# Kernel tuning notes

Measured on AMD Instinct MI355X. Metric: run time of the kernel, lower is better.

The kernel has to match this reference:

```python
import jax, jax.numpy as jnp
import numpy as np

P = 2000
C, H, W = 512, 192, 336
STRIDE = 8
IMG_H, IMG_W = H * STRIDE, W * STRIDE


def setup_inputs() -> dict:
    key = jax.random.key(0)
    kx, kxs, kys = jax.random.split(key, 3)
    x = jax.random.normal(kx, (1, C, H, W), dtype=jnp.float32)
    # valid boxes: x1<=x2 in [0, IMG_W), y1<=y2 in [0, IMG_H)
    xs = jnp.sort(jax.random.randint(kxs, (P, 2), 0, IMG_W), axis=1).astype(jnp.float32)
    ys = jnp.sort(jax.random.randint(kys, (P, 2), 0, IMG_H), axis=1).astype(jnp.float32)
    bbox = jnp.stack([xs[:, 0], ys[:, 0], xs[:, 1], ys[:, 1]], axis=1)  # (P,4) x1,y1,x2,y2
    scale_ratio = jnp.array([float(STRIDE), float(STRIDE)], dtype=jnp.float32)
    return {"x": x, "bbox": bbox, "scale_ratio": scale_ratio, "select_num": 10}


def reference(x, bbox, scale_ratio, select_num):
    # x: [1, C, H, W]. Per-box score = mean of x over (C, y1:y2+1, x1:x2+1).
    # Equivalent: spatial mean over the box of the channel-mean map, computed
    # for all boxes at once via a 2D integral image (summed-area table).
    g = x[0].mean(axis=0)  # [H, W] channel-mean map
    sat = jnp.pad(jnp.cumsum(jnp.cumsum(g, axis=0), axis=1), ((1, 0), (1, 0)))  # [H+1, W+1]

    x1 = jnp.clip(jnp.floor_divide(bbox[:, 0], scale_ratio[1]).astype(jnp.int32), 0, W - 1)
    y1 = jnp.clip(jnp.floor_divide(bbox[:, 1], scale_ratio[0]).astype(jnp.int32), 0, H - 1)
    x2 = jnp.clip(jnp.floor_divide(bbox[:, 2], scale_ratio[1]).astype(jnp.int32), 0, W - 1)
    y2 = jnp.clip(jnp.floor_divide(bbox[:, 3], scale_ratio[0]).astype(jnp.int32), 0, H - 1)

    box_sum = (sat[y2 + 1, x2 + 1] - sat[y1, x2 + 1]
               - sat[y2 + 1, x1] + sat[y1, x1])  # (P,)
    area = ((y2 - y1 + 1) * (x2 - x1 + 1)).astype(x.dtype)
    scores = box_sum / area  # (P,)

    # threshold between the select_num-th and (select_num+1)-th largest (P > select_num)
    top = jax.lax.top_k(scores, select_num + 1)[0]
    thresh = 0.5 * (top[select_num - 1] + top[select_num])
    out = jax.nn.sigmoid((scores - thresh) * 100.0)
    return out.reshape(P, 1, 1, 1)
```

## Files before the change

kernel.cpp:

```cpp
#include <hip/hip_runtime.h>
#include <hip/hip_bf16.h>
#include <math.h>

#define PBOX 2000
#define CC   512
#define HH   192
#define WW   336
#define HWSZ (HH * WW)
#define NCOL4 (HWSZ / 4)
#define SATW 340
#define SATH (HH + 1)

__global__ __launch_bounds__(256) void k_chanmean(const float* __restrict__ x,
                                                  float* __restrict__ g) {
    const int t    = threadIdx.x;
    const int sub  = t >> 5;
    const int o    = t & 31;
    const int col4 = blockIdx.x * 32 + o;

    const float4* __restrict__ x4 = (const float4*)x;
    const int cbase = sub * (CC / 8);

    float4 acc = make_float4(0.f, 0.f, 0.f, 0.f);
#pragma unroll 4
    for (int c = 0; c < CC / 8; ++c) {
        float4 v = x4[(size_t)(cbase + c) * NCOL4 + col4];
        acc.x += v.x; acc.y += v.y; acc.z += v.z; acc.w += v.w;
    }

    __shared__ float4 red[256];
    red[t] = acc;
    __syncthreads();

    if (sub == 0) {
        float4 s = red[o];
#pragma unroll
        for (int k = 1; k < 8; ++k) {
            float4 v = red[k * 32 + o];
            s.x += v.x; s.y += v.y; s.z += v.z; s.w += v.w;
        }
        const float inv = 1.0f / (float)CC;
        s.x *= inv; s.y *= inv; s.z *= inv; s.w *= inv;
        ((float4*)g)[col4] = s;
    }
}

__global__ __launch_bounds__(512) void k_sat(const float* __restrict__ g,
                                             float* __restrict__ sat) {
    const int t = threadIdx.x;

    for (int i = t; i <= WW; i += 512) sat[i] = 0.f;
    for (int i = t; i <= HH; i += 512) sat[(size_t)i * SATW] = 0.f;

    if (t < HH) {
        const float4* __restrict__ g4 = (const float4*)(g + (size_t)t * WW);
        float* __restrict__ sr = sat + (size_t)(t + 1) * SATW + 1;
        float run = 0.f;
        for (int q = 0; q < WW / 4; ++q) {
            float4 v = g4[q];
            float s0 = run + v.x;
            float s1 = s0 + v.y;
            float s2 = s1 + v.z;
            float s3 = s2 + v.w;
            run = s3;
            sr[q * 4 + 0] = s0;
            sr[q * 4 + 1] = s1;
            sr[q * 4 + 2] = s2;
            sr[q * 4 + 3] = s3;
        }
    }
    __syncthreads();

    if (t < WW) {
        float* __restrict__ scp = sat + (t + 1);
        float run = 0.f;
        for (int y = 1; y <= HH; ++y) {
            run += scp[(size_t)y * SATW];
            scp[(size_t)y * SATW] = run;
        }
    }
}

__global__ __launch_bounds__(256) void k_boxes(const float4* __restrict__ bbox,
                                               const float* __restrict__ scale,
                                               const int* __restrict__ selnum,
                                               const float* __restrict__ sat,
                                               float* __restrict__ out) {
    constexpr int TPB = 256;
    constexpr int BPT = 8;
    constexpr int PPAD = TPB * BPT;

    __shared__ float sc[PPAD];
    __shared__ float topv[64];
    __shared__ float wval[4];
    __shared__ int   widx[4];

    const int t = threadIdx.x;
    const float sx = scale[1];
    const float sy = scale[0];

    float myscore[BPT];
#pragma unroll
    for (int i = 0; i < BPT; ++i) {
        const int p = t + i * TPB;
        float score = -INFINITY;
        if (p < PBOX) {
            float4 b = bbox[p];
            int x1 = min(max((int)floorf(b.x / sx), 0), WW - 1);
            int y1 = min(max((int)floorf(b.y / sy), 0), HH - 1);
            int x2 = min(max((int)floorf(b.z / sx), 0), WW - 1);
            int y2 = min(max((int)floorf(b.w / sy), 0), HH - 1);
            float s = sat[(size_t)(y2 + 1) * SATW + (x2 + 1)]
                    - sat[(size_t)y1 * SATW + (x2 + 1)]
                    - sat[(size_t)(y2 + 1) * SATW + x1]
                    + sat[(size_t)y1 * SATW + x1];
            float area = (float)((y2 - y1 + 1) * (x2 - x1 + 1));
            score = s / area;
        }
        myscore[i] = score;
        sc[p < PBOX ? p : (t + i * TPB)] = score;
    }
    __syncthreads();

    const int sn = *selnum;
    const int rounds = min(sn + 1, 64);

    for (int r = 0; r < rounds; ++r) {
        float bv = -INFINITY;
        int bi = 0;
#pragma unroll
        for (int i = 0; i < BPT; ++i) {
            const int p = t + i * TPB;
            const float v = sc[p];
            if (v > bv) { bv = v; bi = p; }
        }
        for (int off = 32; off > 0; off >>= 1) {
            float ov = __shfl_down(bv, off);
            int   oi = __shfl_down(bi, off);
            if (ov > bv) { bv = ov; bi = oi; }
        }
        const int wid = t >> 6;
        if ((t & 63) == 0) { wval[wid] = bv; widx[wid] = bi; }
        __syncthreads();
        if (t == 0) {
            float fv = wval[0]; int fi = widx[0];
#pragma unroll
            for (int w = 1; w < 4; ++w)
                if (wval[w] > fv) { fv = wval[w]; fi = widx[w]; }
            topv[r] = fv;
            sc[fi] = -INFINITY;
        }
        __syncthreads();
    }

    const float thresh = 0.5f * (topv[sn - 1] + topv[sn]);

#pragma unroll
    for (int i = 0; i < BPT; ++i) {
        const int p = t + i * TPB;
        if (p < PBOX) {
            const float z = (myscore[i] - thresh) * 100.0f;
            out[p] = 1.0f / (1.0f + expf(-z));
        }
    }
}

extern "C" void kernel_launch(void* const* d_in, const int* in_sizes, int n_in,
                              void* d_out, int out_size, void* d_ws, size_t ws_size,
                              hipStream_t stream) {
    const float* x     = (const float*)d_in[0];
    const float* bbox  = (const float*)d_in[1];
    const float* scale = (const float*)d_in[2];
    const int*   seln  = (const int*)d_in[3];

    float* g   = (float*)d_ws;
    float* sat = g + HWSZ;

    k_chanmean<<<NCOL4 / 32, 256, 0, stream>>>(x, g);
    k_sat<<<1, 512, 0, stream>>>(g, sat);
    k_boxes<<<1, 256, 0, stream>>>((const float4*)bbox, scale, seln, sat,
                                   (float*)d_out);
}
```

Before: 241.9 us.

## Fuse SAT build with box scoring and single-wavefront top-k selection

Merges the summed-area-table kernel and the box-scoring kernel into one single-block launch, removing a kernel launch and its dependency gap. The top-k selection now runs in one 64-lane wavefront using xor shuffles, which drops the per-round block barriers. The column scan batches 16 loads ahead of the dependent adds, and the loop unroll factors grow. The channel-mean pass dominates the runtime, so the overall effect is likely small.

```diff
diff --git a/kernel.cpp b/kernel.cpp
--- a/kernel.cpp
+++ b/kernel.cpp
@@ -22,7 +22,7 @@
     const int cbase = sub * (CC / 8);
 
     float4 acc = make_float4(0.f, 0.f, 0.f, 0.f);
-#pragma unroll 4
+#pragma unroll 8
     for (int c = 0; c < CC / 8; ++c) {
         float4 v = x4[(size_t)(cbase + c) * NCOL4 + col4];
         acc.x += v.x; acc.y += v.y; acc.z += v.z; acc.w += v.w;
@@ -45,17 +45,27 @@
     }
 }
 
-__global__ __launch_bounds__(512) void k_sat(const float* __restrict__ g,
-                                             float* __restrict__ sat) {
+__global__ __launch_bounds__(512) void k_sat_boxes(const float* __restrict__ g,
+                                                   float* __restrict__ sat,
+                                                   const float4* __restrict__ bbox,
+                                                   const float* __restrict__ scale,
+                                                   const int* __restrict__ selnum,
+                                                   float* __restrict__ out) {
+    constexpr int TPB = 512;
+    constexpr int BPT = 4;
+    __shared__ float sc[TPB * BPT];
+    __shared__ float s_thresh;
+
     const int t = threadIdx.x;
 
-    for (int i = t; i <= WW; i += 512) sat[i] = 0.f;
-    for (int i = t; i <= HH; i += 512) sat[(size_t)i * SATW] = 0.f;
+    for (int i = t; i <= WW; i += TPB) sat[i] = 0.f;
+    for (int i = t; i <= HH; i += TPB) sat[(size_t)i * SATW] = 0.f;
 
     if (t < HH) {
         const float4* __restrict__ g4 = (const float4*)(g + (size_t)t * WW);
         float* __restrict__ sr = sat + (size_t)(t + 1) * SATW + 1;
         float run = 0.f;
+#pragma unroll 4
         for (int q = 0; q < WW / 4; ++q) {
             float4 v = g4[q];
             float s0 = run + v.x;
@@ -74,28 +84,19 @@
     if (t < WW) {
         float* __restrict__ scp = sat + (t + 1);
         float run = 0.f;
-        for (int y = 1; y <= HH; ++y) {
-            run += scp[(size_t)y * SATW];
-            scp[(size_t)y * SATW] = run;
+        for (int y0 = 1; y0 <= HH; y0 += 16) {
+            float v[16];
+#pragma unroll
+            for (int k = 0; k < 16; ++k) v[k] = scp[(size_t)(y0 + k) * SATW];
+#pragma unroll
+            for (int k = 0; k < 16; ++k) {
+                run += v[k];
+                scp[(size_t)(y0 + k) * SATW] = run;
+            }
         }
     }
-}
+    __syncthreads();
 
-__global__ __launch_bounds__(256) void k_boxes(const float4* __restrict__ bbox,
-                                               const float* __restrict__ scale,
-                                               const int* __restrict__ selnum,
-                                               const float* __restrict__ sat,
-                                               float* __restrict__ out) {
-    constexpr int TPB = 256;
-    constexpr int BPT = 8;
-    constexpr int PPAD = TPB * BPT;
-
-    __shared__ float sc[PPAD];
-    __shared__ float topv[64];
-    __shared__ float wval[4];
-    __shared__ int   widx[4];
-
-    const int t = threadIdx.x;
     const float sx = scale[1];
     const float sy = scale[0];
 
@@ -118,43 +119,39 @@
             score = s / area;
         }
         myscore[i] = score;
-        sc[p < PBOX ? p : (t + i * TPB)] = score;
+        sc[p] = score;
     }
     __syncthreads();
 
-    const int sn = *selnum;
-    const int rounds = min(sn + 1, 64);
+    if (t < 64) {
+        const int sn = selnum[0];
+        const int rounds = min(sn + 1, 63);
+        float va = -INFINITY, vb = -INFINITY;
 
-    for (int r = 0; r < rounds; ++r) {
-        float bv = -INFINITY;
-        int bi = 0;
+        for (int r = 0; r < rounds; ++r) {
+            float bv = -INFINITY;
+            int bi = t;
 #pragma unroll
-        for (int i = 0; i < BPT; ++i) {
-            const int p = t + i * TPB;
-            const float v = sc[p];
-            if (v > bv) { bv = v; bi = p; }
+            for (int k = 0; k < (TPB * BPT) / 64; ++k) {
+                const int p = k * 64 + t;
+                const float v = sc[p];
+                if (v > bv) { bv = v; bi = p; }
+            }
+#pragma unroll
+            for (int off = 32; off > 0; off >>= 1) {
+                float ov = __shfl_xor(bv, off);
+                int   oi = __shfl_xor(bi, off);
+                if (ov > bv) { bv = ov; bi = oi; }
+            }
+            if ((bi & 63) == t) sc[bi] = -INFINITY;
+            if (r == sn - 1) va = bv;
+            if (r == sn)     vb = bv;
         }
-        for (int off = 32; off > 0; off >>= 1) {
-            float ov = __shfl_down(bv, off);
-            int   oi = __shfl_down(bi, off);
-            if (ov > bv) { bv = ov; bi = oi; }
-        }
-        const int wid = t >> 6;
-        if ((t & 63) == 0) { wval[wid] = bv; widx[wid] = bi; }
-        __syncthreads();
-        if (t == 0) {
-            float fv = wval[0]; int fi = widx[0];
-#pragma unroll
-            for (int w = 1; w < 4; ++w)
-                if (wval[w] > fv) { fv = wval[w]; fi = widx[w]; }
-            topv[r] = fv;
-            sc[fi] = -INFINITY;
-        }
-        __syncthreads();
+        if (t == 0) s_thresh = 0.5f * (va + vb);
     }
+    __syncthreads();
 
-    const float thresh = 0.5f * (topv[sn - 1] + topv[sn]);
-
+    const float thresh = s_thresh;
 #pragma unroll
     for (int i = 0; i < BPT; ++i) {
         const int p = t + i * TPB;
@@ -177,7 +174,6 @@
     float* sat = g + HWSZ;
 
     k_chanmean<<<NCOL4 / 32, 256, 0, stream>>>(x, g);
-    k_sat<<<1, 512, 0, stream>>>(g, sat);
-    k_boxes<<<1, 256, 0, stream>>>((const float4*)bbox, scale, seln, sat,
-                                   (float*)d_out);
+    k_sat_boxes<<<1, 512, 0, stream>>>(g, sat, (const float4*)bbox, scale, seln,
+                                       (float*)d_out);
 }
```

After: 240.3 us. Within noise of the previous version (-0.7%).
